# Performance work log

Measured on AMD Instinct MI355X. Metric: run time of the kernel, lower is better.

## Reference

```python
import jax, jax.numpy as jnp
import numpy as np

N = 100000      # nodes
E = 1600000     # edges (avg degree 16)
DIN = 128       # in_feats
H = 4           # num_heads
D = 32          # out_feats per head
NEG_SLOPE = 0.2


def setup_inputs() -> dict:
    key = jax.random.key(0)
    k1, k2, k3, k4, k5, k6 = jax.random.split(key, 6)
    feat = jax.random.normal(k1, (N, DIN), dtype=jnp.float32)
    src = jax.random.randint(k2, (E,), 0, N, dtype=jnp.int32)
    dst = jax.random.randint(k3, (E,), 0, N, dtype=jnp.int32)
    # learned params (fc kernel + attention vectors)
    W = jax.random.normal(k4, (DIN, H * D), dtype=jnp.float32) * 0.05
    attn_l = jax.random.normal(k5, (H, D), dtype=jnp.float32) * 0.05
    attn_r = jax.random.normal(k6, (H, D), dtype=jnp.float32) * 0.05
    return {"feat": feat, "src": src, "dst": dst, "W": W,
            "attn_l": attn_l, "attn_r": attn_r}


def reference(feat, src, dst, W, attn_l, attn_r):
    # linear projection: (N, DIN) @ (DIN, H*D) -> (N, H, D)
    h = (feat @ W).reshape(N, H, D)
    # per-node attention half-logits: (N, H)
    el = jnp.einsum("nhd,hd->nh", h, attn_l)
    er = jnp.einsum("nhd,hd->nh", h, attn_r)
    # edge-wise logits e_ij = LeakyReLU(el[src] + er[dst]) : (E, H)
    e = jax.nn.leaky_relu(el[src] + er[dst], negative_slope=NEG_SLOPE)
    # segment softmax over incoming edges of each dst node
    emax = jax.ops.segment_max(e, dst, num_segments=N)          # (N, H)
    emax = jnp.where(jnp.isfinite(emax), emax, 0.0)             # empty segs
    ee = jnp.exp(e - emax[dst])                                 # (E, H)
    denom = jax.ops.segment_sum(ee, dst, num_segments=N)        # (N, H)
    a = ee / denom[dst]                                         # (E, H)
    # weighted message + scatter-sum aggregation: (N, H, D)
    msg = h[src] * a[:, :, None]                                # (E, H, D)
    out = jax.ops.segment_sum(msg, dst, num_segments=N)
    return out
```

## Files before the change

### kernel.cpp

```cpp
#include <hip/hip_runtime.h>
#include <hip/hip_fp16.h>

#define N_NODES 100000
#define N_EDGES 1600000
#define DIN 128
#define NH 4
#define ND 32
#define HD 128
#define NEG_SLOPE 0.2f
#define MROWS 64
#define APAD 136
#define GEMM_BLOCKS ((N_NODES + MROWS - 1) / MROWS)

#define NBUCK 782
#define CHB 8192
#define NHB 196
#define WCONV_BLOCKS 64

typedef _Float16 half8_t __attribute__((ext_vector_type(8)));
typedef float f32x4 __attribute__((ext_vector_type(4)));

__device__ __forceinline__ float lrelu(float x) {
    return x > 0.0f ? x : NEG_SLOPE * x;
}

union Pack8  { uint2 u; __half2 h2[2]; };
union Pack16 { uint4 u; __half2 h2[4]; };

__global__ __launch_bounds__(256) void k_histw(
    const int* __restrict__ dst, int* __restrict__ hist,
    const float* __restrict__ W, __half* __restrict__ Wt) {
    __shared__ int cnt[NBUCK];
    const int tid = threadIdx.x;

    if ((int)blockIdx.x >= NHB) {
        int i = (blockIdx.x - NHB) * 256 + tid;
        int k = i >> 7, c = i & 127;
        Wt[c * DIN + k] = __float2half(W[k * HD + c]);
        return;
    }
    if (!hist) return;
    for (int i = tid; i < NBUCK; i += 256) cnt[i] = 0;
    __syncthreads();
    int base = blockIdx.x * CHB;
#pragma unroll
    for (int j = 0; j < CHB / 256; ++j) {
        int e = base + j * 256 + tid;
        if (e < N_EDGES) atomicAdd(&cnt[dst[e] >> 7], 1);
    }
    __syncthreads();
    int* hrow = hist + (size_t)blockIdx.x * NBUCK;
    for (int i = tid; i < NBUCK; i += 256) hrow[i] = cnt[i];
}

__global__ __launch_bounds__(256) void k_scanH(int* __restrict__ hist,
                                               int* __restrict__ tot) {
    __shared__ int wtot[4];
    int b = blockIdx.x, tid = threadIdx.x;
    int v = (tid < NHB) ? hist[(size_t)tid * NBUCK + b] : 0;
    int lane = tid & 63, wv = tid >> 6;
    int incl = v;
#pragma unroll
    for (int off = 1; off < 64; off <<= 1) {
        int t = __shfl_up(incl, off, 64);
        if (lane >= off) incl += t;
    }
    if (lane == 63) wtot[wv] = incl;
    __syncthreads();
    int woff = 0;
    for (int w = 0; w < wv; ++w) woff += wtot[w];
    if (tid < NHB) hist[(size_t)tid * NBUCK + b] = woff + incl - v;
    if (tid == 0) tot[b] = wtot[0] + wtot[1] + wtot[2] + wtot[3];
}

__global__ __launch_bounds__(256) void k_scanT(const int* __restrict__ tot,
                                               int* __restrict__ bucket_base,
                                               int* __restrict__ rowptr) {
    __shared__ int wtot[4];
    int tid = threadIdx.x;
    int idx0 = tid * 4;
    int v[4];
#pragma unroll
    for (int j = 0; j < 4; ++j) {
        int b = idx0 + j;
        v[j] = (b < NBUCK) ? tot[b] : 0;
    }
    int s = v[0] + v[1] + v[2] + v[3];
    int lane = tid & 63;
    int incl = s;
#pragma unroll
    for (int off = 1; off < 64; off <<= 1) {
        int t = __shfl_up(incl, off, 64);
        if (lane >= off) incl += t;
    }
    if (lane == 63) wtot[tid >> 6] = incl;
    __syncthreads();
    int woff = 0;
    for (int w = 0; w < (tid >> 6); ++w) woff += wtot[w];
    int run = woff + incl - s;
#pragma unroll
    for (int j = 0; j < 4; ++j) {
        int b = idx0 + j;
        if (b < NBUCK) {
            int old = v[j];
            bucket_base[b] = run;
            run += old;
        }
    }
    if (tid == 0) {
        int total = wtot[0] + wtot[1] + wtot[2] + wtot[3];
        bucket_base[NBUCK] = total;
        rowptr[N_NODES] = total;
    }
}

__global__ __launch_bounds__(256) void k_gemmcscat(
    const float* __restrict__ feat, const __half* __restrict__ Wt,
    const float* __restrict__ attn_l, const float* __restrict__ attn_r,
    __half* __restrict__ hhalf, float* __restrict__ el, float* __restrict__ er,
    const int* __restrict__ src, const int* __restrict__ dst,
    const int* __restrict__ hist, const int* __restrict__ bucket_base,
    int* __restrict__ bucketed) {

    __shared__ __align__(16) __half As[MROWS * APAD];
    __shared__ __align__(16) __half Bs[HD * APAD];

    const int tid = threadIdx.x;

    if ((int)blockIdx.x < NHB) {
        if (!bucketed) return;
        int* cur = (int*)As;
        const int* hrow = hist + (size_t)blockIdx.x * NBUCK;
        for (int i = tid; i < NBUCK; i += 256) cur[i] = bucket_base[i] + hrow[i];
        __syncthreads();
        int base = blockIdx.x * CHB;
#pragma unroll
        for (int j = 0; j < CHB / 256; ++j) {
            int e = base + j * 256 + tid;
            if (e < N_EDGES) {
                int d = dst[e];
                int slot = atomicAdd(&cur[d >> 7], 1);
                bucketed[slot] = src[e] | ((d & 127) << 17);
            }
        }
        return;
    }

    const int row0 = (blockIdx.x - NHB) * MROWS;

    {
        const uint4* Wv = (const uint4*)Wt;
#pragma unroll
        for (int i = 0; i < 8; ++i) {
            int idx = tid + i * 256;
            int c = idx >> 4, k8 = idx & 15;
            *(uint4*)(&Bs[c * APAD + k8 * 8]) = Wv[idx];
        }
    }
    {
#pragma unroll
        for (int i = 0; i < 8; ++i) {
            int idx = tid + i * 256;
            int r = idx >> 5, c4 = idx & 31;
            int row = row0 + r;
            float4 f = (row < N_NODES)
                ? *(const float4*)(feat + (size_t)row * DIN + c4 * 4)
                : make_float4(0.0f, 0.0f, 0.0f, 0.0f);
            Pack8 pk;
            pk.h2[0] = __floats2half2_rn(f.x, f.y);
            pk.h2[1] = __floats2half2_rn(f.z, f.w);
            *(uint2*)(&As[r * APAD + c4 * 4]) = pk.u;
        }
    }
    __syncthreads();

    const int l = tid & 63;
    const int wv = tid >> 6;
    const int lrow = l & 15;
    const int kid = l >> 4;

    f32x4 acc[8];
#pragma unroll
    for (int n = 0; n < 8; ++n) acc[n] = (f32x4){0.0f, 0.0f, 0.0f, 0.0f};

#pragma unroll
    for (int kb = 0; kb < 4; ++kb) {
        half8_t a = *(const half8_t*)(&As[(wv * 16 + lrow) * APAD + kb * 32 + kid * 8]);
#pragma unroll
        for (int n = 0; n < 8; ++n) {
            half8_t b = *(const half8_t*)(&Bs[(n * 16 + lrow) * APAD + kb * 32 + kid * 8]);
            acc[n] = __builtin_amdgcn_mfma_f32_16x16x32_f16(a, b, acc[n], 0, 0, 0);
        }
    }

    __syncthreads();
#pragma unroll
    for (int n = 0; n < 8; ++n)
#pragma unroll
        for (int r = 0; r < 4; ++r)
            As[(wv * 16 + kid * 4 + r) * APAD + n * 16 + lrow] =
                __float2half(acc[n][r]);
    __syncthreads();

    {
        int lr = tid >> 2;
        int row = row0 + lr;
        int head = tid & 3;
        if (row < N_NODES) {
            float suml = 0.0f, sumr = 0.0f;
#pragma unroll
            for (int q = 0; q < 4; ++q) {
                Pack16 p;
                p.u = *(const uint4*)(&As[lr * APAD + head * 32 + q * 8]);
                float4 al0 = *(const float4*)(attn_l + head * 32 + q * 8);
                float4 al1 = *(const float4*)(attn_l + head * 32 + q * 8 + 4);
                float4 ar0 = *(const float4*)(attn_r + head * 32 + q * 8);
                float4 ar1 = *(const float4*)(attn_r + head * 32 + q * 8 + 4);
                float2 x0 = __half22float2(p.h2[0]);
                float2 x1 = __half22float2(p.h2[1]);
                float2 x2 = __half22float2(p.h2[2]);
                float2 x3 = __half22float2(p.h2[3]);
                suml += x0.x * al0.x + x0.y * al0.y + x1.x * al0.z + x1.y * al0.w;
                suml += x2.x * al1.x + x2.y * al1.y + x3.x * al1.z + x3.y * al1.w;
                sumr += x0.x * ar0.x + x0.y * ar0.y + x1.x * ar0.z + x1.y * ar0.w;
                sumr += x2.x * ar1.x + x2.y * ar1.y + x3.x * ar1.z + x3.y * ar1.w;
                *(uint4*)(hhalf + (size_t)row * HD + head * 32 + q * 8) = p.u;
            }
            el[(size_t)row * NH + head] = suml;
            er[(size_t)row * NH + head] = sumr;
        }
    }
}

__global__ __launch_bounds__(256) void k_fine(
    const int* __restrict__ bucketed, const int* __restrict__ bbase,
    int* __restrict__ srcs, int* __restrict__ rowptr) {

    __shared__ int cnt[128];
    __shared__ int noff[129];
    __shared__ int cur[128];

    const int b = blockIdx.x;
    const int tid = threadIdx.x;
    const int node0 = b << 7;
    const int beg = bbase[b], end = bbase[b + 1];

    if (tid < 128) cnt[tid] = 0;
    __syncthreads();

    for (int e = beg + tid; e < end; e += 256)
        atomicAdd(&cnt[bucketed[e] >> 17], 1);
    __syncthreads();

    if (tid < 64) {
        int v0 = cnt[tid * 2], v1 = cnt[tid * 2 + 1];
        int s = v0 + v1;
        int incl = s;
#pragma unroll
        for (int off = 1; off < 64; off <<= 1) {
            int t = __shfl_up(incl, off, 64);
            if (tid >= off) incl += t;
        }
        int excl = incl - s;
        noff[tid * 2] = excl;
        noff[tid * 2 + 1] = excl + v0;
        cur[tid * 2] = excl;
        cur[tid * 2 + 1] = excl + v0;
        if (tid == 63) noff[128] = incl;
    }
    __syncthreads();

    if (tid < 128) {
        int node = node0 + tid;
        if (node < N_NODES) rowptr[node] = beg + noff[tid];
    }

    for (int e = beg + tid; e < end; e += 256) {
        int p = bucketed[e];
        int d7 = p >> 17;
        int slot = beg + atomicAdd(&cur[d7], 1);
        srcs[slot] = p & 0x1FFFF;
    }
}

__global__ __launch_bounds__(256) void k_agg_csr(
    const int* __restrict__ rowptr, const int* __restrict__ srcs,
    const float* __restrict__ el, const float* __restrict__ er,
    const __half* __restrict__ hhalf, float* __restrict__ out) {
    int node = blockIdx.x * 4 + (threadIdx.x >> 6);
    int lane = threadIdx.x & 63;
    int grp = lane >> 4;
    int cl = lane & 15;
    int head = cl >> 2;
    int beg = rowptr[node], end = rowptr[node + 1];

    const float er_h = er[(size_t)node * NH + head];

    float dsum = 0.0f;
    float a[8];
#pragma unroll
    for (int q = 0; q < 8; ++q) a[q] = 0.0f;

    int i = beg + grp;
    for (; i + 12 < end; i += 16) {
        int s0 = srcs[i], s1 = srcs[i + 4], s2 = srcs[i + 8], s3 = srcs[i + 12];
        float e0 = el[(size_t)s0 * NH + head];
        float e1 = el[(size_t)s1 * NH + head];
        float e2 = el[(size_t)s2 * NH + head];
        float e3 = el[(size_t)s3 * NH + head];
        Pack16 p0, p1, p2, p3;
        p0.u = *(const uint4*)(hhalf + (size_t)s0 * HD + cl * 8);
        p1.u = *(const uint4*)(hhalf + (size_t)s1 * HD + cl * 8);
        p2.u = *(const uint4*)(hhalf + (size_t)s2 * HD + cl * 8);
        p3.u = *(const uint4*)(hhalf + (size_t)s3 * HD + cl * 8);
        float w0 = __expf(lrelu(e0 + er_h));
        float w1 = __expf(lrelu(e1 + er_h));
        float w2 = __expf(lrelu(e2 + er_h));
        float w3 = __expf(lrelu(e3 + er_h));
        dsum += (w0 + w1) + (w2 + w3);
#pragma unroll
        for (int q = 0; q < 4; ++q) {
            float2 x0 = __half22float2(p0.h2[q]);
            float2 x1 = __half22float2(p1.h2[q]);
            float2 x2 = __half22float2(p2.h2[q]);
            float2 x3 = __half22float2(p3.h2[q]);
            a[2 * q]     = fmaf(x0.x, w0, a[2 * q]);
            a[2 * q + 1] = fmaf(x0.y, w0, a[2 * q + 1]);
            a[2 * q]     = fmaf(x1.x, w1, a[2 * q]);
            a[2 * q + 1] = fmaf(x1.y, w1, a[2 * q + 1]);
            a[2 * q]     = fmaf(x2.x, w2, a[2 * q]);
            a[2 * q + 1] = fmaf(x2.y, w2, a[2 * q + 1]);
            a[2 * q]     = fmaf(x3.x, w3, a[2 * q]);
            a[2 * q + 1] = fmaf(x3.y, w3, a[2 * q + 1]);
        }
    }
    for (; i + 4 < end; i += 8) {
        int s0 = srcs[i], s1 = srcs[i + 4];
        float e0 = el[(size_t)s0 * NH + head];
        float e1 = el[(size_t)s1 * NH + head];
        Pack16 p0, p1;
        p0.u = *(const uint4*)(hhalf + (size_t)s0 * HD + cl * 8);
        p1.u = *(const uint4*)(hhalf + (size_t)s1 * HD + cl * 8);
        float w0 = __expf(lrelu(e0 + er_h));
        float w1 = __expf(lrelu(e1 + er_h));
        dsum += w0 + w1;
#pragma unroll
        for (int q = 0; q < 4; ++q) {
            float2 x0 = __half22float2(p0.h2[q]);
            float2 x1 = __half22float2(p1.h2[q]);
            a[2 * q]     = fmaf(x0.x, w0, a[2 * q]);
            a[2 * q + 1] = fmaf(x0.y, w0, a[2 * q + 1]);
            a[2 * q]     = fmaf(x1.x, w1, a[2 * q]);
            a[2 * q + 1] = fmaf(x1.y, w1, a[2 * q + 1]);
        }
    }
    if (i < end) {
        int s0 = srcs[i];
        float w0 = __expf(lrelu(el[(size_t)s0 * NH + head] + er_h));
        Pack16 p0;
        p0.u = *(const uint4*)(hhalf + (size_t)s0 * HD + cl * 8);
        dsum += w0;
#pragma unroll
        for (int q = 0; q < 4; ++q) {
            float2 x0 = __half22float2(p0.h2[q]);
            a[2 * q]     = fmaf(x0.x, w0, a[2 * q]);
            a[2 * q + 1] = fmaf(x0.y, w0, a[2 * q + 1]);
        }
    }

    dsum += __shfl_xor(dsum, 16, 64);
    dsum += __shfl_xor(dsum, 32, 64);
#pragma unroll
    for (int q = 0; q < 8; ++q) {
        a[q] += __shfl_xor(a[q], 16, 64);
        a[q] += __shfl_xor(a[q], 32, 64);
    }

    if (grp == 0) {
        float inv = (end > beg) ? 1.0f / dsum : 0.0f;
        *(float4*)(out + (size_t)node * HD + cl * 8) =
            make_float4(a[0] * inv, a[1] * inv, a[2] * inv, a[3] * inv);
        *(float4*)(out + (size_t)node * HD + cl * 8 + 4) =
            make_float4(a[4] * inv, a[5] * inv, a[6] * inv, a[7] * inv);
    }
}

__global__ void k_init_fb(float* __restrict__ out, float* __restrict__ denom) {
    int i = blockIdx.x * blockDim.x + threadIdx.x;
    int stride = gridDim.x * blockDim.x;
    for (int j = i; j < N_NODES * HD; j += stride) out[j] = 0.0f;
    for (int j = i; j < N_NODES * NH; j += stride) denom[j] = 0.0f;
}

__global__ __launch_bounds__(256) void k_denom_fb(
    const int* __restrict__ src, const int* __restrict__ dst,
    const float* __restrict__ el, const float* __restrict__ er,
    float* __restrict__ denom) {
    int e = blockIdx.x * blockDim.x + threadIdx.x;
    if (e >= N_EDGES) return;
    int s = src[e], d = dst[e];
    float4 l = *(const float4*)(el + (size_t)s * NH);
    float4 r = *(const float4*)(er + (size_t)d * NH);
    float* dn = denom + (size_t)d * NH;
    atomicAdd(dn + 0, __expf(lrelu(l.x + r.x)));
    atomicAdd(dn + 1, __expf(lrelu(l.y + r.y)));
    atomicAdd(dn + 2, __expf(lrelu(l.z + r.z)));
    atomicAdd(dn + 3, __expf(lrelu(l.w + r.w)));
}

__global__ __launch_bounds__(256) void k_agg_fb(
    const int* __restrict__ src, const int* __restrict__ dst,
    const float* __restrict__ el, const float* __restrict__ er,
    const float* __restrict__ denom, const __half* __restrict__ hhalf,
    float* __restrict__ out) {
    long long t = (long long)blockIdx.x * blockDim.x + threadIdx.x;
    if (t >= (long long)N_EDGES * HD) return;
    int e = (int)(t >> 7);
    int c = (int)(t & 127);
    int hh = c >> 5;
    int s = src[e], d = dst[e];
    float x = lrelu(el[(size_t)s * NH + hh] + er[(size_t)d * NH + hh]);
    float a = __expf(x) / denom[(size_t)d * NH + hh];
    atomicAdd(out + (size_t)d * HD + c,
              __half2float(hhalf[(size_t)s * HD + c]) * a);
}

extern "C" void kernel_launch(void* const* d_in, const int* in_sizes, int n_in,
                              void* d_out, int out_size, void* d_ws, size_t ws_size,
                              hipStream_t stream) {
    const float* feat   = (const float*)d_in[0];
    const int*   src    = (const int*)d_in[1];
    const int*   dst    = (const int*)d_in[2];
    const float* W      = (const float*)d_in[3];
    const float* attn_l = (const float*)d_in[4];
    const float* attn_r = (const float*)d_in[5];
    float* out = (float*)d_out;

    char* base = (char*)d_ws;
    size_t off = 0;
    auto take = [&](size_t bytes) -> char* {
        char* r = base + off;
        off = (off + bytes + 255) & ~(size_t)255;
        return r;
    };
    __half* hhalf  = (__half*)take((size_t)N_NODES * HD * 2);
    float* el      = (float*)take((size_t)N_NODES * NH * 4);
    float* er      = (float*)take((size_t)N_NODES * NH * 4);
    __half* Wt     = (__half*)take((size_t)DIN * HD * 2);
    int*  hist     = (int*)take((size_t)NHB * NBUCK * 4);
    int*  tot      = (int*)take((size_t)NBUCK * 4);
    int*  bbase    = (int*)take((size_t)(NBUCK + 1) * 4);
    int*  bucketed = (int*)take((size_t)N_EDGES * 4);
    int*  srcs     = (int*)take((size_t)N_EDGES * 4);
    int*  rowptr   = (int*)take((size_t)(N_NODES + 1) * 4);
    float* denom   = (float*)take((size_t)N_NODES * NH * 4);
    bool csr = (off <= ws_size);

    if (csr) {
        k_histw<<<NHB + WCONV_BLOCKS, 256, 0, stream>>>(dst, hist, W, Wt);
        k_scanH<<<NBUCK, 256, 0, stream>>>(hist, tot);
        k_scanT<<<1, 256, 0, stream>>>(tot, bbase, rowptr);
        k_gemmcscat<<<NHB + GEMM_BLOCKS, 256, 0, stream>>>(
            feat, Wt, attn_l, attn_r, hhalf, el, er,
            src, dst, hist, bbase, bucketed);
        k_fine<<<NBUCK, 256, 0, stream>>>(bucketed, bbase, srcs, rowptr);
        k_agg_csr<<<N_NODES / 4, 256, 0, stream>>>(rowptr, srcs, el, er,
                                                   hhalf, out);
    } else {
        int eb = (N_EDGES + 255) / 256;
        k_init_fb<<<2048, 256, 0, stream>>>(out, denom);
        k_histw<<<NHB + WCONV_BLOCKS, 256, 0, stream>>>(dst, (int*)nullptr, W, Wt);
        k_gemmcscat<<<NHB + GEMM_BLOCKS, 256, 0, stream>>>(
            feat, Wt, attn_l, attn_r, hhalf, el, er,
            src, dst, (const int*)nullptr, (const int*)nullptr, (int*)nullptr);
        k_denom_fb<<<eb, 256, 0, stream>>>(src, dst, el, er, denom);
        long long totw = (long long)N_EDGES * HD;
        int ab = (int)((totw + 255) / 256);
        k_agg_fb<<<ab, 256, 0, stream>>>(src, dst, el, er, denom, hhalf, out);
    }
}
```

Before: 145.8 us.

## Fuse bucket scans with last-block pattern and retune histogram chunking

Merges the per-bucket column scan and the single-block total scan into one kernel. The last block to finish, detected with an atomic counter and thread fences, does the final scan, which removes one kernel launch and the dependency gap before it. The counter is reset inside the histogram kernel. Histogram chunk size is lowered so more blocks share the edge count, and the fine-sort kernel moves to 512 threads per block. The cost is atomics and fences in every scan block and extra per-bucket scan work, since each now covers up to 250 rows.

```diff
diff --git a/kernel.cpp b/kernel.cpp
--- a/kernel.cpp
+++ b/kernel.cpp
@@ -13,8 +13,8 @@
 #define GEMM_BLOCKS ((N_NODES + MROWS - 1) / MROWS)
 
 #define NBUCK 782
-#define CHB 8192
-#define NHB 196
+#define CHB 6400
+#define NHB 250
 #define WCONV_BLOCKS 64
 
 typedef _Float16 half8_t __attribute__((ext_vector_type(8)));
@@ -29,11 +29,13 @@
 
 __global__ __launch_bounds__(256) void k_histw(
     const int* __restrict__ dst, int* __restrict__ hist,
-    const float* __restrict__ W, __half* __restrict__ Wt) {
+    const float* __restrict__ W, __half* __restrict__ Wt,
+    int* __restrict__ done) {
     __shared__ int cnt[NBUCK];
     const int tid = threadIdx.x;
 
     if ((int)blockIdx.x >= NHB) {
+        if (blockIdx.x == NHB && tid == 0 && done) *done = 0;
         int i = (blockIdx.x - NHB) * 256 + tid;
         int k = i >> 7, c = i & 127;
         Wt[c * DIN + k] = __float2half(W[k * HD + c]);
@@ -53,9 +55,11 @@
     for (int i = tid; i < NBUCK; i += 256) hrow[i] = cnt[i];
 }
 
-__global__ __launch_bounds__(256) void k_scanH(int* __restrict__ hist,
-                                               int* __restrict__ tot) {
+__global__ __launch_bounds__(256) void k_scanHT(
+    int* __restrict__ hist, int* __restrict__ tot, int* __restrict__ done,
+    int* __restrict__ bucket_base, int* __restrict__ rowptr) {
     __shared__ int wtot[4];
+    __shared__ int lastFlag;
     int b = blockIdx.x, tid = threadIdx.x;
     int v = (tid < NHB) ? hist[(size_t)tid * NBUCK + b] : 0;
     int lane = tid & 63, wv = tid >> 6;
@@ -70,40 +74,43 @@
     int woff = 0;
     for (int w = 0; w < wv; ++w) woff += wtot[w];
     if (tid < NHB) hist[(size_t)tid * NBUCK + b] = woff + incl - v;
-    if (tid == 0) tot[b] = wtot[0] + wtot[1] + wtot[2] + wtot[3];
-}
-
-__global__ __launch_bounds__(256) void k_scanT(const int* __restrict__ tot,
-                                               int* __restrict__ bucket_base,
-                                               int* __restrict__ rowptr) {
-    __shared__ int wtot[4];
-    int tid = threadIdx.x;
+    if (tid == 0)
+        atomicExch(&tot[b], wtot[0] + wtot[1] + wtot[2] + wtot[3]);
+
+    __threadfence();
+    if (tid == 0) {
+        int prev = atomicAdd(done, 1);
+        lastFlag = (prev == NBUCK - 1);
+    }
+    __syncthreads();
+    if (!lastFlag) return;
+    __threadfence();
+
     int idx0 = tid * 4;
-    int v[4];
+    int v4[4];
 #pragma unroll
     for (int j = 0; j < 4; ++j) {
-        int b = idx0 + j;
-        v[j] = (b < NBUCK) ? tot[b] : 0;
-    }
-    int s = v[0] + v[1] + v[2] + v[3];
-    int lane = tid & 63;
-    int incl = s;
+        int bb = idx0 + j;
+        v4[j] = (bb < NBUCK) ? atomicAdd(&tot[bb], 0) : 0;
+    }
+    int s = v4[0] + v4[1] + v4[2] + v4[3];
+    int incl2 = s;
 #pragma unroll
     for (int off = 1; off < 64; off <<= 1) {
-        int t = __shfl_up(incl, off, 64);
-        if (lane >= off) incl += t;
-    }
-    if (lane == 63) wtot[tid >> 6] = incl;
-    __syncthreads();
-    int woff = 0;
-    for (int w = 0; w < (tid >> 6); ++w) woff += wtot[w];
-    int run = woff + incl - s;
+        int t = __shfl_up(incl2, off, 64);
+        if (lane >= off) incl2 += t;
+    }
+    if (lane == 63) wtot[wv] = incl2;
+    __syncthreads();
+    int woff2 = 0;
+    for (int w = 0; w < wv; ++w) woff2 += wtot[w];
+    int run = woff2 + incl2 - s;
 #pragma unroll
     for (int j = 0; j < 4; ++j) {
-        int b = idx0 + j;
-        if (b < NBUCK) {
-            int old = v[j];
-            bucket_base[b] = run;
+        int bb = idx0 + j;
+        if (bb < NBUCK) {
+            int old = v4[j];
+            bucket_base[bb] = run;
             run += old;
         }
     }
@@ -232,7 +239,7 @@
     }
 }
 
-__global__ __launch_bounds__(256) void k_fine(
+__global__ __launch_bounds__(512) void k_fine(
     const int* __restrict__ bucketed, const int* __restrict__ bbase,
     int* __restrict__ srcs, int* __restrict__ rowptr) {
 
@@ -248,7 +255,7 @@
     if (tid < 128) cnt[tid] = 0;
     __syncthreads();
 
-    for (int e = beg + tid; e < end; e += 256)
+    for (int e = beg + tid; e < end; e += 512)
         atomicAdd(&cnt[bucketed[e] >> 17], 1);
     __syncthreads();
 
@@ -275,7 +282,7 @@
         if (node < N_NODES) rowptr[node] = beg + noff[tid];
     }
 
-    for (int e = beg + tid; e < end; e += 256) {
+    for (int e = beg + tid; e < end; e += 512) {
         int p = bucketed[e];
         int d7 = p >> 17;
         int slot = beg + atomicAdd(&cur[d7], 1);
@@ -449,6 +456,7 @@
     __half* Wt     = (__half*)take((size_t)DIN * HD * 2);
     int*  hist     = (int*)take((size_t)NHB * NBUCK * 4);
     int*  tot      = (int*)take((size_t)NBUCK * 4);
+    int*  done     = (int*)take(256);
     int*  bbase    = (int*)take((size_t)(NBUCK + 1) * 4);
     int*  bucketed = (int*)take((size_t)N_EDGES * 4);
     int*  srcs     = (int*)take((size_t)N_EDGES * 4);
@@ -457,19 +465,19 @@
     bool csr = (off <= ws_size);
 
     if (csr) {
-        k_histw<<<NHB + WCONV_BLOCKS, 256, 0, stream>>>(dst, hist, W, Wt);
-        k_scanH<<<NBUCK, 256, 0, stream>>>(hist, tot);
-        k_scanT<<<1, 256, 0, stream>>>(tot, bbase, rowptr);
+        k_histw<<<NHB + WCONV_BLOCKS, 256, 0, stream>>>(dst, hist, W, Wt, done);
+        k_scanHT<<<NBUCK, 256, 0, stream>>>(hist, tot, done, bbase, rowptr);
         k_gemmcscat<<<NHB + GEMM_BLOCKS, 256, 0, stream>>>(
             feat, Wt, attn_l, attn_r, hhalf, el, er,
             src, dst, hist, bbase, bucketed);
-        k_fine<<<NBUCK, 256, 0, stream>>>(bucketed, bbase, srcs, rowptr);
+        k_fine<<<NBUCK, 512, 0, stream>>>(bucketed, bbase, srcs, rowptr);
         k_agg_csr<<<N_NODES / 4, 256, 0, stream>>>(rowptr, srcs, el, er,
                                                    hhalf, out);
     } else {
         int eb = (N_EDGES + 255) / 256;
         k_init_fb<<<2048, 256, 0, stream>>>(out, denom);
-        k_histw<<<NHB + WCONV_BLOCKS, 256, 0, stream>>>(dst, (int*)nullptr, W, Wt);
+        k_histw<<<NHB + WCONV_BLOCKS, 256, 0, stream>>>(dst, (int*)nullptr,
+                                                        W, Wt, (int*)nullptr);
         k_gemmcscat<<<NHB + GEMM_BLOCKS, 256, 0, stream>>>(
             feat, Wt, attn_l, attn_r, hhalf, el, er,
             src, dst, (const int*)nullptr, (const int*)nullptr, (int*)nullptr);
```

Result: slower. 261.7 us (+79.5%).
